# Kernel optimization log

Hardware: AMD Instinct MI355X
Metric: run time of the kernel (lower is better)

Reference implementation:

```python
import jax, jax.numpy as jnp
import numpy as np

B, O, T, C_IN, IMG, P, D = 16, 3, 8, 3, 224, 16, 768
HF = IMG // P  # 14x14 conv feature grid
S = 7          # ObjectsCrops output size (SxS per object per frame)


def setup_inputs() -> dict:
    key = jax.random.key(0)
    ks = jax.random.split(key, 6)
    x = jax.random.normal(ks[0], (B, C_IN, T, IMG, IMG), dtype=jnp.float32)
    # metadata: [B, O, T, 4] boxes (x1,y1,x2,y2) in pixel coords within [0,224]
    u = jax.random.uniform(ks[1], (B, O, T, 4), dtype=jnp.float32)
    bx1 = u[..., 0] * 160.0
    by1 = u[..., 1] * 160.0
    bw = 16.0 + u[..., 2] * 48.0
    bh = 16.0 + u[..., 3] * 48.0
    metadata = jnp.stack([bx1, by1, jnp.minimum(bx1 + bw, 224.0), jnp.minimum(by1 + bh, 224.0)], axis=-1)
    proj_w = jax.random.normal(ks[2], (D, C_IN, P, P), dtype=jnp.float32) * 0.02  # Conv3d kernel, tubelet dim (=1) squeezed
    proj_b = jnp.zeros((D,), dtype=jnp.float32)
    box_categories = jax.random.normal(ks[3], (T, O, D), dtype=jnp.float32) * 0.02
    w1 = jax.random.normal(ks[4], (4, D // 2), dtype=jnp.float32) * 0.1   # Linear(4, 384, bias=False)
    w2 = jax.random.normal(ks[5], (D // 2, D), dtype=jnp.float32) * 0.05  # Linear(384, 768, bias=False)
    return dict(x=x, metadata=metadata, proj_w=proj_w, proj_b=proj_b, box_categories=box_categories, w1=w1, w2=w2)


def _roi_crop(feat, boxes):
    # feat: [BT, C, Hf, Wf]; boxes: [BT, O, 4] (x1,y1,x2,y2) in feature-map coords
    BT, C, Hf, Wf = feat.shape
    x1, y1, x2, y2 = (boxes[..., i] for i in range(4))
    cell = (jnp.arange(S, dtype=feat.dtype) + 0.5) / S               # sample cell centers
    ys = y1[..., None] + cell * (y2 - y1)[..., None]                 # [BT,O,S]
    xs = x1[..., None] + cell * (x2 - x1)[..., None]
    yg = jnp.broadcast_to(ys[:, :, :, None], (BT, O, S, S)) - 0.5    # pixel centers at idx+0.5
    xg = jnp.broadcast_to(xs[:, :, None, :], (BT, O, S, S)) - 0.5
    y0f = jnp.floor(yg); x0f = jnp.floor(xg)
    wy = yg - y0f; wx = xg - x0f
    y0 = jnp.clip(y0f.astype(jnp.int32), 0, Hf - 1); y1i = jnp.clip(y0 + 1, 0, Hf - 1)
    x0 = jnp.clip(x0f.astype(jnp.int32), 0, Wf - 1); x1i = jnp.clip(x0 + 1, 0, Wf - 1)
    gather = jax.vmap(lambda fm, yy, xx: fm[:, yy, xx])              # [C,Hf,Wf],[O,S,S] -> [C,O,S,S]
    v00 = gather(feat, y0, x0); v01 = gather(feat, y0, x1i)
    v10 = gather(feat, y1i, x0); v11 = gather(feat, y1i, x1i)
    wy = wy[:, None]; wx = wx[:, None]                               # [BT,1,O,S,S]
    return (v00 * (1 - wy) * (1 - wx) + v01 * (1 - wy) * wx
            + v10 * wy * (1 - wx) + v11 * wy * wx)                   # [BT,C,O,S,S]


def reference(x, metadata, proj_w, proj_b, box_categories, w1, w2):
    Bs = x.shape[0]
    boxes = jnp.transpose(metadata, (0, 2, 1, 3))                    # [B,T,O,4] pixel coords
    # coordinate MLP on normalized boxes + per-(frame,object) category embedding
    box_emb = jax.nn.relu(jax.nn.relu((boxes / 224.0) @ w1) @ w2)    # [B,T,O,D]
    box_emb = box_categories[None] + box_emb
    # Conv3d patch embed: tubelet=1, stride==kernel -> non-overlapping patchify + GEMM
    xp = x.reshape(Bs, C_IN, T, HF, P, HF, P)
    feat = jnp.einsum('bcthpwq,dcpq->btdhw', xp, proj_w) + proj_b[None, None, :, None, None]
    feat = feat.reshape(Bs * T, D, HF, HF)
    fboxes = boxes.reshape(Bs * T, O, 4) * (HF / 224.0)              # boxes in feature coords
    crops = _roi_crop(feat, fboxes).reshape(Bs, T, D, O, S, S)
    xo = jnp.transpose(crops, (0, 3, 2, 1, 4, 5))                    # [B,O,C,T,S,S]
    emb = jnp.transpose(box_emb, (0, 2, 3, 1))                       # [B,O,D,T]
    xo = xo + emb[..., None, None]
    xo = xo.reshape(Bs * O, D, T, S * S)                             # flatten(3) on [N*O,C,T,H,W]
    return jnp.transpose(xo, (0, 2, 3, 1))                           # [B*O, T, S*S, D]
```

## Files before the change

kernel.cpp:

```cpp
#include <hip/hip_runtime.h>
#include <hip/hip_bf16.h>

typedef unsigned int u32;
typedef unsigned short ushort_t;
typedef __bf16 bf16x8 __attribute__((ext_vector_type(8)));
typedef float f32x4 __attribute__((ext_vector_type(4)));
typedef unsigned short ushort8 __attribute__((ext_vector_type(8)));

#define GM 25088
#define GK 768
#define GN 768

__device__ __forceinline__ ushort_t f2bf(float f) {
    u32 u = __float_as_uint(f);
    u32 r = (u + 0x7FFFu + ((u >> 16) & 1u)) >> 16;
    return (ushort_t)r;
}

__device__ __forceinline__ void load_lds16(const void* g, void* l) {
    __builtin_amdgcn_global_load_lds(
        (const __attribute__((address_space(1))) u32*)g,
        (__attribute__((address_space(3))) u32*)l, 16, 0, 0);
}

__global__ __launch_bounds__(256) void pack_a(const float* __restrict__ x,
                                              ushort_t* __restrict__ Ap) {
    int g = blockIdx.x * 256 + threadIdx.x;
    int w = g % 14;
    int rowg = g / 14;
    int row = rowg % 224;
    int bct = rowg / 224;
    int t = bct % 8;
    int bc = bct / 8;
    int c = bc % 3;
    int b = bc / 3;
    int p = row & 15;
    int h = row >> 4;
    const float* src = x + (size_t)g * 16;
    f32x4 f0 = *(const f32x4*)src;
    f32x4 f1 = *(const f32x4*)(src + 4);
    f32x4 f2 = *(const f32x4*)(src + 8);
    f32x4 f3 = *(const f32x4*)(src + 12);
    ushort8 r0, r1;
    r0[0] = f2bf(f0[0]); r0[1] = f2bf(f0[1]); r0[2] = f2bf(f0[2]); r0[3] = f2bf(f0[3]);
    r0[4] = f2bf(f1[0]); r0[5] = f2bf(f1[1]); r0[6] = f2bf(f1[2]); r0[7] = f2bf(f1[3]);
    r1[0] = f2bf(f2[0]); r1[1] = f2bf(f2[1]); r1[2] = f2bf(f2[2]); r1[3] = f2bf(f2[3]);
    r1[4] = f2bf(f3[0]); r1[5] = f2bf(f3[1]); r1[6] = f2bf(f3[2]); r1[7] = f2bf(f3[3]);
    int m = ((b * 8 + t) * 14 + h) * 14 + w;
    int k = c * 256 + p * 16;
    *(ushort8*)(Ap + (size_t)m * 768 + k) = r0;
    *(ushort8*)(Ap + (size_t)m * 768 + k + 8) = r1;
}

__global__ __launch_bounds__(256) void pack_w(const float* __restrict__ w,
                                              ushort_t* __restrict__ Wp) {
    size_t g = ((size_t)blockIdx.x * 256 + threadIdx.x) * 8;
    f32x4 f0 = *(const f32x4*)(w + g);
    f32x4 f1 = *(const f32x4*)(w + g + 4);
    ushort8 r;
    r[0] = f2bf(f0[0]); r[1] = f2bf(f0[1]); r[2] = f2bf(f0[2]); r[3] = f2bf(f0[3]);
    r[4] = f2bf(f1[0]); r[5] = f2bf(f1[1]); r[6] = f2bf(f1[2]); r[7] = f2bf(f1[3]);
    *(ushort8*)(Wp + g) = r;
}

__global__ __launch_bounds__(256) void box_mlp(const float* __restrict__ meta,
                                               const float* __restrict__ w1,
                                               const float* __restrict__ w2,
                                               const float* __restrict__ cats,
                                               float* __restrict__ emb) {
    int bt = blockIdx.x / 3;
    int dc = blockIdx.x % 3;
    int b = bt / 8, t = bt % 8;
    __shared__ float H[3][384];
    int tid = threadIdx.x;
    for (int idx = tid; idx < 3 * 384; idx += 256) {
        int o = idx / 384, j = idx % 384;
        const float* mp = meta + ((b * 3 + o) * 8 + t) * 4;
        float s = 0.f;
        #pragma unroll
        for (int i = 0; i < 4; ++i) s += (mp[i] * (1.0f / 224.0f)) * w1[i * 384 + j];
        H[o][j] = fmaxf(s, 0.f);
    }
    __syncthreads();
    int d = dc * 256 + tid;
    float acc[3] = {0.f, 0.f, 0.f};
    #pragma unroll 4
    for (int j = 0; j < 384; ++j) {
        float wv = w2[j * 768 + d];
        acc[0] += H[0][j] * wv;
        acc[1] += H[1][j] * wv;
        acc[2] += H[2][j] * wv;
    }
    #pragma unroll
    for (int o = 0; o < 3; ++o) {
        emb[((size_t)bt * 3 + o) * 768 + d] =
            fmaxf(acc[o], 0.f) + cats[(t * 3 + o) * 768 + d];
    }
}

__global__ __launch_bounds__(256) void gemm_bt(const ushort_t* __restrict__ A,
                                               const ushort_t* __restrict__ Bt,
                                               const float* __restrict__ pb,
                                               float* __restrict__ C) {
    __shared__ ushort_t lA[128 * 64];
    __shared__ ushort_t lB[128 * 64];
    int tid = threadIdx.x;
    int bid = blockIdx.x;
    int wid = (bid & 7) * 147 + (bid >> 3);
    int bm = wid / 6;
    int bn = wid % 6;
    size_t m0 = (size_t)bm * 128, n0 = (size_t)bn * 128;
    int w = tid >> 6, lane = tid & 63;
    int wr = w >> 1, wc = w & 1;

    f32x4 acc[4][4] = {};

    for (int kt = 0; kt < 12; ++kt) {
        int k0 = kt * 64;
        __syncthreads();
        #pragma unroll
        for (int r = 0; r < 4; ++r) {
            int cidx = r * 256 + tid;
            int row = cidx >> 3;
            int col = (cidx & 7) * 8;
            load_lds16(A + ((m0 + row) * 768 + k0 + col), &lA[(size_t)cidx * 8]);
        }
        #pragma unroll
        for (int r = 0; r < 4; ++r) {
            int cidx = r * 256 + tid;
            int row = cidx >> 3;
            int col = (cidx & 7) * 8;
            load_lds16(Bt + ((n0 + row) * 768 + k0 + col), &lB[(size_t)cidx * 8]);
        }
        __syncthreads();
        #pragma unroll
        for (int kk = 0; kk < 2; ++kk) {
            bf16x8 af[4], bfr[4];
            #pragma unroll
            for (int mi = 0; mi < 4; ++mi)
                af[mi] = *(const bf16x8*)&lA[(wr * 64 + mi * 16 + (lane & 15)) * 64
                                             + kk * 32 + (lane >> 4) * 8];
            #pragma unroll
            for (int ni = 0; ni < 4; ++ni)
                bfr[ni] = *(const bf16x8*)&lB[(wc * 64 + ni * 16 + (lane & 15)) * 64
                                              + kk * 32 + (lane >> 4) * 8];
            #pragma unroll
            for (int mi = 0; mi < 4; ++mi)
                #pragma unroll
                for (int ni = 0; ni < 4; ++ni)
                    acc[mi][ni] = __builtin_amdgcn_mfma_f32_16x16x32_bf16(
                        af[mi], bfr[ni], acc[mi][ni], 0, 0, 0);
        }
    }

    int rbase = (lane >> 4) * 4;
    int cl = lane & 15;
    #pragma unroll
    for (int ni = 0; ni < 4; ++ni) {
        size_t col = n0 + wc * 64 + ni * 16 + cl;
        float pbv = pb[col];
        #pragma unroll
        for (int mi = 0; mi < 4; ++mi) {
            size_t row = m0 + wr * 64 + mi * 16 + rbase;
            #pragma unroll
            for (int j = 0; j < 4; ++j) {
                C[(row + j) * 768 + col] = acc[mi][ni][j] + pbv;
            }
        }
    }
}

__global__ __launch_bounds__(192) void roi_kernel(const float* __restrict__ meta,
                                                  const float* __restrict__ feat,
                                                  const float* __restrict__ emb,
                                                  float* __restrict__ out) {
    int bid = blockIdx.x;
    int wid = (bid & 7) * 336 + (bid >> 3);
    int i = wid % 7; wid /= 7;
    int o = wid % 3; wid /= 3;
    int t = wid % 8;
    int b = wid / 8;

    const float* mp = meta + ((b * 3 + o) * 8 + t) * 4;
    float x1 = mp[0] * (1.f / 16.f);
    float y1 = mp[1] * (1.f / 16.f);
    float x2 = mp[2] * (1.f / 16.f);
    float y2 = mp[3] * (1.f / 16.f);

    float ci = (i + 0.5f) * (1.f / 7.f);
    float yg = y1 + ci * (y2 - y1) - 0.5f;
    float y0f = floorf(yg);
    float wy = yg - y0f;
    int y0 = min(max((int)y0f, 0), 13);
    int y1c = min(y0 + 1, 13);

    int bt = b * 8 + t;
    const float* fbase = feat + (size_t)bt * 196 * 768;
    const float* ep = emb + ((size_t)bt * 3 + o) * 768;

    int d = threadIdx.x * 4;
    f32x4 ev = *(const f32x4*)(ep + d);

    for (int j = 0; j < 7; ++j) {
        float cj = (j + 0.5f) * (1.f / 7.f);
        float xgv = x1 + cj * (x2 - x1) - 0.5f;
        float x0f = floorf(xgv);
        float wx = xgv - x0f;
        int x0 = min(max((int)x0f, 0), 13);
        int x1i = min(x0 + 1, 13);

        f32x4 v00 = *(const f32x4*)(fbase + ((size_t)y0 * 14 + x0) * 768 + d);
        f32x4 v01 = *(const f32x4*)(fbase + ((size_t)y0 * 14 + x1i) * 768 + d);
        f32x4 v10 = *(const f32x4*)(fbase + ((size_t)y1c * 14 + x0) * 768 + d);
        f32x4 v11 = *(const f32x4*)(fbase + ((size_t)y1c * 14 + x1i) * 768 + d);

        float w00 = (1.f - wy) * (1.f - wx);
        float w01 = (1.f - wy) * wx;
        float w10 = wy * (1.f - wx);
        float w11 = wy * wx;

        f32x4 r;
        #pragma unroll
        for (int e = 0; e < 4; ++e)
            r[e] = v00[e] * w00 + v01[e] * w01 + v10[e] * w10 + v11[e] * w11 + ev[e];

        int pp = i * 7 + j;
        *(f32x4*)(out + ((((size_t)(b * 3 + o) * 8 + t) * 49 + pp) * 768 + d)) = r;
    }
}

extern "C" void kernel_launch(void* const* d_in, const int* in_sizes, int n_in,
                              void* d_out, int out_size, void* d_ws, size_t ws_size,
                              hipStream_t stream) {
    const float* x     = (const float*)d_in[0];
    const float* meta  = (const float*)d_in[1];
    const float* projw = (const float*)d_in[2];
    const float* projb = (const float*)d_in[3];
    const float* cats  = (const float*)d_in[4];
    const float* w1    = (const float*)d_in[5];
    const float* w2    = (const float*)d_in[6];
    float* out = (float*)d_out;

    char* ws = (char*)d_ws;
    const size_t szA = (size_t)GM * GK * 2;
    const size_t szW = (size_t)GN * GK * 2;
    const size_t szF = (size_t)GM * GN * 4;
    ushort_t* Ap   = (ushort_t*)(ws);
    ushort_t* Wp   = (ushort_t*)(ws + szA);
    float*    feat = (float*)(ws + szA + szW);
    float*    emb  = (float*)(ws + szA + szW + szF);

    pack_a<<<4704, 256, 0, stream>>>(x, Ap);
    pack_w<<<288, 256, 0, stream>>>(projw, Wp);
    box_mlp<<<128 * 3, 256, 0, stream>>>(meta, w1, w2, cats, emb);
    gemm_bt<<<1176, 256, 0, stream>>>(Ap, Wp, projb, feat);
    roi_kernel<<<2688, 192, 0, stream>>>(meta, feat, emb, out);
}
```

Measured before the change: 270.5 us.

## Fuse prep kernels, double-buffer swizzled GEMM, store bf16 features, persistent ROI

```diff
diff --git a/kernel.cpp b/kernel.cpp
--- a/kernel.cpp
+++ b/kernel.cpp
@@ -6,6 +6,7 @@
 typedef __bf16 bf16x8 __attribute__((ext_vector_type(8)));
 typedef float f32x4 __attribute__((ext_vector_type(4)));
 typedef unsigned short ushort8 __attribute__((ext_vector_type(8)));
+typedef unsigned short ushort4v __attribute__((ext_vector_type(4)));
 
 #define GM 25088
 #define GK 768
@@ -17,93 +18,118 @@
     return (ushort_t)r;
 }
 
+__device__ __forceinline__ f32x4 bf2f4(ushort4v u) {
+    f32x4 f;
+    #pragma unroll
+    for (int e = 0; e < 4; ++e) f[e] = __uint_as_float(((u32)u[e]) << 16);
+    return f;
+}
+
 __device__ __forceinline__ void load_lds16(const void* g, void* l) {
     __builtin_amdgcn_global_load_lds(
         (const __attribute__((address_space(1))) u32*)g,
         (__attribute__((address_space(3))) u32*)l, 16, 0, 0);
 }
 
-__global__ __launch_bounds__(256) void pack_a(const float* __restrict__ x,
-                                              ushort_t* __restrict__ Ap) {
-    int g = blockIdx.x * 256 + threadIdx.x;
-    int w = g % 14;
-    int rowg = g / 14;
-    int row = rowg % 224;
-    int bct = rowg / 224;
-    int t = bct % 8;
-    int bc = bct / 8;
-    int c = bc % 3;
-    int b = bc / 3;
-    int p = row & 15;
-    int h = row >> 4;
-    const float* src = x + (size_t)g * 16;
-    f32x4 f0 = *(const f32x4*)src;
-    f32x4 f1 = *(const f32x4*)(src + 4);
-    f32x4 f2 = *(const f32x4*)(src + 8);
-    f32x4 f3 = *(const f32x4*)(src + 12);
-    ushort8 r0, r1;
-    r0[0] = f2bf(f0[0]); r0[1] = f2bf(f0[1]); r0[2] = f2bf(f0[2]); r0[3] = f2bf(f0[3]);
-    r0[4] = f2bf(f1[0]); r0[5] = f2bf(f1[1]); r0[6] = f2bf(f1[2]); r0[7] = f2bf(f1[3]);
-    r1[0] = f2bf(f2[0]); r1[1] = f2bf(f2[1]); r1[2] = f2bf(f2[2]); r1[3] = f2bf(f2[3]);
-    r1[4] = f2bf(f3[0]); r1[5] = f2bf(f3[1]); r1[6] = f2bf(f3[2]); r1[7] = f2bf(f3[3]);
-    int m = ((b * 8 + t) * 14 + h) * 14 + w;
-    int k = c * 256 + p * 16;
-    *(ushort8*)(Ap + (size_t)m * 768 + k) = r0;
-    *(ushort8*)(Ap + (size_t)m * 768 + k + 8) = r1;
-}
-
-__global__ __launch_bounds__(256) void pack_w(const float* __restrict__ w,
-                                              ushort_t* __restrict__ Wp) {
-    size_t g = ((size_t)blockIdx.x * 256 + threadIdx.x) * 8;
-    f32x4 f0 = *(const f32x4*)(w + g);
-    f32x4 f1 = *(const f32x4*)(w + g + 4);
-    ushort8 r;
-    r[0] = f2bf(f0[0]); r[1] = f2bf(f0[1]); r[2] = f2bf(f0[2]); r[3] = f2bf(f0[3]);
-    r[4] = f2bf(f1[0]); r[5] = f2bf(f1[1]); r[6] = f2bf(f1[2]); r[7] = f2bf(f1[3]);
-    *(ushort8*)(Wp + g) = r;
-}
-
-__global__ __launch_bounds__(256) void box_mlp(const float* __restrict__ meta,
-                                               const float* __restrict__ w1,
-                                               const float* __restrict__ w2,
-                                               const float* __restrict__ cats,
-                                               float* __restrict__ emb) {
-    int bt = blockIdx.x / 3;
-    int dc = blockIdx.x % 3;
-    int b = bt / 8, t = bt % 8;
+__global__ __launch_bounds__(256) void prep(const float* __restrict__ x,
+                                            const float* __restrict__ projw,
+                                            const float* __restrict__ meta,
+                                            const float* __restrict__ w1,
+                                            const float* __restrict__ w2,
+                                            const float* __restrict__ cats,
+                                            ushort_t* __restrict__ Ap,
+                                            ushort_t* __restrict__ Wp,
+                                            float* __restrict__ emb) {
     __shared__ float H[3][384];
+    int bid = blockIdx.x;
     int tid = threadIdx.x;
-    for (int idx = tid; idx < 3 * 384; idx += 256) {
-        int o = idx / 384, j = idx % 384;
-        const float* mp = meta + ((b * 3 + o) * 8 + t) * 4;
-        float s = 0.f;
-        #pragma unroll
-        for (int i = 0; i < 4; ++i) s += (mp[i] * (1.0f / 224.0f)) * w1[i * 384 + j];
-        H[o][j] = fmaxf(s, 0.f);
-    }
-    __syncthreads();
-    int d = dc * 256 + tid;
-    float acc[3] = {0.f, 0.f, 0.f};
-    #pragma unroll 4
-    for (int j = 0; j < 384; ++j) {
-        float wv = w2[j * 768 + d];
-        acc[0] += H[0][j] * wv;
-        acc[1] += H[1][j] * wv;
-        acc[2] += H[2][j] * wv;
-    }
-    #pragma unroll
-    for (int o = 0; o < 3; ++o) {
-        emb[((size_t)bt * 3 + o) * 768 + d] =
-            fmaxf(acc[o], 0.f) + cats[(t * 3 + o) * 768 + d];
+    if (bid < 1176) {
+        int g = bid * 256 + tid;
+        int m = g / 12;
+        int piece = g % 12;
+        int w = m % 14, h = (m / 14) % 14, t = (m / 196) % 8, b = m / 1568;
+        int c = piece >> 2, p0 = (piece & 3) * 4;
+        const float* src = x + ((size_t)((b * 3 + c) * 8 + t) * 224 + h * 16 + p0) * 224 + w * 16;
+        int xo = (m & 7) << 4;
+        ushort_t* dst = Ap + (size_t)m * 768 + piece * 64;
+        #pragma unroll
+        for (int i = 0; i < 4; ++i) {
+            const float* s = src + i * 224;
+            f32x4 f0 = *(const f32x4*)(s);
+            f32x4 f1 = *(const f32x4*)(s + 4);
+            f32x4 f2 = *(const f32x4*)(s + 8);
+            f32x4 f3 = *(const f32x4*)(s + 12);
+            ushort8 r0, r1;
+            r0[0] = f2bf(f0[0]); r0[1] = f2bf(f0[1]); r0[2] = f2bf(f0[2]); r0[3] = f2bf(f0[3]);
+            r0[4] = f2bf(f1[0]); r0[5] = f2bf(f1[1]); r0[6] = f2bf(f1[2]); r0[7] = f2bf(f1[3]);
+            r1[0] = f2bf(f2[0]); r1[1] = f2bf(f2[1]); r1[2] = f2bf(f2[2]); r1[3] = f2bf(f2[3]);
+            r1[4] = f2bf(f3[0]); r1[5] = f2bf(f3[1]); r1[6] = f2bf(f3[2]); r1[7] = f2bf(f3[3]);
+            int b0 = (i * 32) ^ xo;
+            int b1 = (i * 32 + 16) ^ xo;
+            *(ushort8*)(dst + (b0 >> 1)) = r0;
+            *(ushort8*)(dst + (b1 >> 1)) = r1;
+        }
+    } else if (bid < 1212) {
+        int g = (bid - 1176) * 256 + tid;
+        int n = g / 12;
+        int piece = g % 12;
+        const float* src = projw + (size_t)n * 768 + piece * 64;
+        int xo = (n & 7) << 4;
+        ushort_t* dst = Wp + (size_t)n * 768 + piece * 64;
+        #pragma unroll
+        for (int i = 0; i < 4; ++i) {
+            const float* s = src + i * 16;
+            f32x4 f0 = *(const f32x4*)(s);
+            f32x4 f1 = *(const f32x4*)(s + 4);
+            f32x4 f2 = *(const f32x4*)(s + 8);
+            f32x4 f3 = *(const f32x4*)(s + 12);
+            ushort8 r0, r1;
+            r0[0] = f2bf(f0[0]); r0[1] = f2bf(f0[1]); r0[2] = f2bf(f0[2]); r0[3] = f2bf(f0[3]);
+            r0[4] = f2bf(f1[0]); r0[5] = f2bf(f1[1]); r0[6] = f2bf(f1[2]); r0[7] = f2bf(f1[3]);
+            r1[0] = f2bf(f2[0]); r1[1] = f2bf(f2[1]); r1[2] = f2bf(f2[2]); r1[3] = f2bf(f2[3]);
+            r1[4] = f2bf(f3[0]); r1[5] = f2bf(f3[1]); r1[6] = f2bf(f3[2]); r1[7] = f2bf(f3[3]);
+            int b0 = (i * 32) ^ xo;
+            int b1 = (i * 32 + 16) ^ xo;
+            *(ushort8*)(dst + (b0 >> 1)) = r0;
+            *(ushort8*)(dst + (b1 >> 1)) = r1;
+        }
+    } else {
+        int bb = bid - 1212;
+        int bt = bb / 3;
+        int dc = bb % 3;
+        int b = bt / 8, t = bt % 8;
+        for (int idx = tid; idx < 3 * 384; idx += 256) {
+            int o = idx / 384, j = idx % 384;
+            const float* mp = meta + ((b * 3 + o) * 8 + t) * 4;
+            float s = 0.f;
+            #pragma unroll
+            for (int i = 0; i < 4; ++i) s += (mp[i] * (1.0f / 224.0f)) * w1[i * 384 + j];
+            H[o][j] = fmaxf(s, 0.f);
+        }
+        __syncthreads();
+        int d = dc * 256 + tid;
+        float acc[3] = {0.f, 0.f, 0.f};
+        #pragma unroll 4
+        for (int j = 0; j < 384; ++j) {
+            float wv = w2[j * 768 + d];
+            acc[0] += H[0][j] * wv;
+            acc[1] += H[1][j] * wv;
+            acc[2] += H[2][j] * wv;
+        }
+        #pragma unroll
+        for (int o = 0; o < 3; ++o) {
+            emb[((size_t)bt * 3 + o) * 768 + d] =
+                fmaxf(acc[o], 0.f) + cats[(t * 3 + o) * 768 + d];
+        }
     }
 }
 
 __global__ __launch_bounds__(256) void gemm_bt(const ushort_t* __restrict__ A,
                                                const ushort_t* __restrict__ Bt,
                                                const float* __restrict__ pb,
-                                               float* __restrict__ C) {
-    __shared__ ushort_t lA[128 * 64];
-    __shared__ ushort_t lB[128 * 64];
+                                               ushort_t* __restrict__ Cb) {
+    __shared__ ushort_t lA[2][128 * 64];
+    __shared__ ushort_t lB[2][128 * 64];
     int tid = threadIdx.x;
     int bid = blockIdx.x;
     int wid = (bid & 7) * 147 + (bid >> 3);
@@ -112,38 +138,46 @@
     size_t m0 = (size_t)bm * 128, n0 = (size_t)bn * 128;
     int w = tid >> 6, lane = tid & 63;
     int wr = w >> 1, wc = w & 1;
+    int r15 = lane & 15;
+    int xoU = (lane & 7) << 3;
 
     f32x4 acc[4][4] = {};
 
+    #define STAGE(buf, kt_)                                                        \
+        {                                                                          \
+            int k0_ = (kt_) * 64;                                                  \
+            _Pragma("unroll")                                                      \
+            for (int r = 0; r < 4; ++r) {                                          \
+                int cidx = r * 256 + tid;                                          \
+                int row = cidx >> 3;                                               \
+                int col = (cidx & 7) * 8;                                          \
+                load_lds16(A + ((m0 + row) * 768 + k0_ + col), &lA[buf][cidx * 8]);\
+            }                                                                      \
+            _Pragma("unroll")                                                      \
+            for (int r = 0; r < 4; ++r) {                                          \
+                int cidx = r * 256 + tid;                                          \
+                int row = cidx >> 3;                                               \
+                int col = (cidx & 7) * 8;                                          \
+                load_lds16(Bt + ((n0 + row) * 768 + k0_ + col), &lB[buf][cidx * 8]);\
+            }                                                                      \
+        }
+
+    STAGE(0, 0);
+    __syncthreads();
+
     for (int kt = 0; kt < 12; ++kt) {
-        int k0 = kt * 64;
-        __syncthreads();
-        #pragma unroll
-        for (int r = 0; r < 4; ++r) {
-            int cidx = r * 256 + tid;
-            int row = cidx >> 3;
-            int col = (cidx & 7) * 8;
-            load_lds16(A + ((m0 + row) * 768 + k0 + col), &lA[(size_t)cidx * 8]);
-        }
-        #pragma unroll
-        for (int r = 0; r < 4; ++r) {
-            int cidx = r * 256 + tid;
-            int row = cidx >> 3;
-            int col = (cidx & 7) * 8;
-            load_lds16(Bt + ((n0 + row) * 768 + k0 + col), &lB[(size_t)cidx * 8]);
-        }
-        __syncthreads();
+        int cur = kt & 1;
+        if (kt < 11) STAGE(cur ^ 1, kt + 1);
         #pragma unroll
         for (int kk = 0; kk < 2; ++kk) {
+            int cs = (kk * 32 + (lane >> 4) * 8) ^ xoU;
             bf16x8 af[4], bfr[4];
             #pragma unroll
             for (int mi = 0; mi < 4; ++mi)
-                af[mi] = *(const bf16x8*)&lA[(wr * 64 + mi * 16 + (lane & 15)) * 64
-                                             + kk * 32 + (lane >> 4) * 8];
+                af[mi] = *(const bf16x8*)&lA[cur][(wr * 64 + mi * 16 + r15) * 64 + cs];
             #pragma unroll
             for (int ni = 0; ni < 4; ++ni)
-                bfr[ni] = *(const bf16x8*)&lB[(wc * 64 + ni * 16 + (lane & 15)) * 64
-                                              + kk * 32 + (lane >> 4) * 8];
+                bfr[ni] = *(const bf16x8*)&lB[cur][(wc * 64 + ni * 16 + r15) * 64 + cs];
             #pragma unroll
             for (int mi = 0; mi < 4; ++mi)
                 #pragma unroll
@@ -151,81 +185,86 @@
                     acc[mi][ni] = __builtin_amdgcn_mfma_f32_16x16x32_bf16(
                         af[mi], bfr[ni], acc[mi][ni], 0, 0, 0);
         }
-    }
+        __syncthreads();
+    }
+    #undef STAGE
 
     int rbase = (lane >> 4) * 4;
-    int cl = lane & 15;
     #pragma unroll
     for (int ni = 0; ni < 4; ++ni) {
-        size_t col = n0 + wc * 64 + ni * 16 + cl;
+        size_t col = n0 + wc * 64 + ni * 16 + r15;
         float pbv = pb[col];
         #pragma unroll
         for (int mi = 0; mi < 4; ++mi) {
             size_t row = m0 + wr * 64 + mi * 16 + rbase;
             #pragma unroll
             for (int j = 0; j < 4; ++j) {
-                C[(row + j) * 768 + col] = acc[mi][ni][j] + pbv;
+                Cb[(row + j) * 768 + col] = f2bf(acc[mi][ni][j] + pbv);
             }
         }
     }
 }
 
 __global__ __launch_bounds__(192) void roi_kernel(const float* __restrict__ meta,
-                                                  const float* __restrict__ feat,
+                                                  const ushort_t* __restrict__ featB,
                                                   const float* __restrict__ emb,
                                                   float* __restrict__ out) {
-    int bid = blockIdx.x;
-    int wid = (bid & 7) * 336 + (bid >> 3);
-    int i = wid % 7; wid /= 7;
-    int o = wid % 3; wid /= 3;
-    int t = wid % 8;
-    int b = wid / 8;
-
-    const float* mp = meta + ((b * 3 + o) * 8 + t) * 4;
-    float x1 = mp[0] * (1.f / 16.f);
-    float y1 = mp[1] * (1.f / 16.f);
-    float x2 = mp[2] * (1.f / 16.f);
-    float y2 = mp[3] * (1.f / 16.f);
-
-    float ci = (i + 0.5f) * (1.f / 7.f);
-    float yg = y1 + ci * (y2 - y1) - 0.5f;
-    float y0f = floorf(yg);
-    float wy = yg - y0f;
-    int y0 = min(max((int)y0f, 0), 13);
-    int y1c = min(y0 + 1, 13);
-
-    int bt = b * 8 + t;
-    const float* fbase = feat + (size_t)bt * 196 * 768;
-    const float* ep = emb + ((size_t)bt * 3 + o) * 768;
-
+    int xcd = blockIdx.x & 7;
+    int idx = blockIdx.x >> 3;
     int d = threadIdx.x * 4;
-    f32x4 ev = *(const f32x4*)(ep + d);
-
-    for (int j = 0; j < 7; ++j) {
-        float cj = (j + 0.5f) * (1.f / 7.f);
-        float xgv = x1 + cj * (x2 - x1) - 0.5f;
-        float x0f = floorf(xgv);
-        float wx = xgv - x0f;
-        int x0 = min(max((int)x0f, 0), 13);
-        int x1i = min(x0 + 1, 13);
-
-        f32x4 v00 = *(const f32x4*)(fbase + ((size_t)y0 * 14 + x0) * 768 + d);
-        f32x4 v01 = *(const f32x4*)(fbase + ((size_t)y0 * 14 + x1i) * 768 + d);
-        f32x4 v10 = *(const f32x4*)(fbase + ((size_t)y1c * 14 + x0) * 768 + d);
-        f32x4 v11 = *(const f32x4*)(fbase + ((size_t)y1c * 14 + x1i) * 768 + d);
-
-        float w00 = (1.f - wy) * (1.f - wx);
-        float w01 = (1.f - wy) * wx;
-        float w10 = wy * (1.f - wx);
-        float w11 = wy * wx;
-
-        f32x4 r;
-        #pragma unroll
-        for (int e = 0; e < 4; ++e)
-            r[e] = v00[e] * w00 + v01[e] * w01 + v10[e] * w10 + v11[e] * w11 + ev[e];
-
-        int pp = i * 7 + j;
-        *(f32x4*)(out + ((((size_t)(b * 3 + o) * 8 + t) * 49 + pp) * 768 + d)) = r;
+
+    for (int wi = idx; wi < 336; wi += 96) {
+        int wid = xcd * 336 + wi;
+        int i = wid % 7; int r = wid / 7;
+        int o = r % 3; r /= 3;
+        int t = r % 8;
+        int b = r / 8;
+
+        const float* mp = meta + ((b * 3 + o) * 8 + t) * 4;
+        float x1 = mp[0] * (1.f / 16.f);
+        float y1 = mp[1] * (1.f / 16.f);
+        float x2 = mp[2] * (1.f / 16.f);
+        float y2 = mp[3] * (1.f / 16.f);
+
+        float ci = (i + 0.5f) * (1.f / 7.f);
+        float yg = y1 + ci * (y2 - y1) - 0.5f;
+        float y0f = floorf(yg);
+        float wy = yg - y0f;
+        int y0 = min(max((int)y0f, 0), 13);
+        int y1c = min(y0 + 1, 13);
+
+        int bt = b * 8 + t;
+        const ushort_t* fbase = featB + (size_t)bt * 196 * 768;
+        const float* ep = emb + ((size_t)bt * 3 + o) * 768;
+        f32x4 ev = *(const f32x4*)(ep + d);
+
+        #pragma unroll
+        for (int j = 0; j < 7; ++j) {
+            float cj = (j + 0.5f) * (1.f / 7.f);
+            float xgv = x1 + cj * (x2 - x1) - 0.5f;
+            float x0f = floorf(xgv);
+            float wx = xgv - x0f;
+            int x0 = min(max((int)x0f, 0), 13);
+            int x1i = min(x0 + 1, 13);
+
+            f32x4 v00 = bf2f4(*(const ushort4v*)(fbase + ((size_t)y0 * 14 + x0) * 768 + d));
+            f32x4 v01 = bf2f4(*(const ushort4v*)(fbase + ((size_t)y0 * 14 + x1i) * 768 + d));
+            f32x4 v10 = bf2f4(*(const ushort4v*)(fbase + ((size_t)y1c * 14 + x0) * 768 + d));
+            f32x4 v11 = bf2f4(*(const ushort4v*)(fbase + ((size_t)y1c * 14 + x1i) * 768 + d));
+
+            float w00 = (1.f - wy) * (1.f - wx);
+            float w01 = (1.f - wy) * wx;
+            float w10 = wy * (1.f - wx);
+            float w11 = wy * wx;
+
+            f32x4 rr;
+            #pragma unroll
+            for (int e = 0; e < 4; ++e)
+                rr[e] = v00[e] * w00 + v01[e] * w01 + v10[e] * w10 + v11[e] * w11 + ev[e];
+
+            int pp = i * 7 + j;
+            *(f32x4*)(out + ((((size_t)(b * 3 + o) * 8 + t) * 49 + pp) * 768 + d)) = rr;
+        }
     }
 }
 
@@ -242,17 +281,15 @@
     float* out = (float*)d_out;
 
     char* ws = (char*)d_ws;
-    const size_t szA = (size_t)GM * GK * 2;
-    const size_t szW = (size_t)GN * GK * 2;
-    const size_t szF = (size_t)GM * GN * 4;
-    ushort_t* Ap   = (ushort_t*)(ws);
-    ushort_t* Wp   = (ushort_t*)(ws + szA);
-    float*    feat = (float*)(ws + szA + szW);
-    float*    emb  = (float*)(ws + szA + szW + szF);
-
-    pack_a<<<4704, 256, 0, stream>>>(x, Ap);
-    pack_w<<<288, 256, 0, stream>>>(projw, Wp);
-    box_mlp<<<128 * 3, 256, 0, stream>>>(meta, w1, w2, cats, emb);
-    gemm_bt<<<1176, 256, 0, stream>>>(Ap, Wp, projb, feat);
-    roi_kernel<<<2688, 192, 0, stream>>>(meta, feat, emb, out);
-}
+    const size_t szA  = (size_t)GM * GK * 2;
+    const size_t szW  = (size_t)GN * GK * 2;
+    const size_t szFB = (size_t)GM * GN * 2;
+    ushort_t* Ap    = (ushort_t*)(ws);
+    ushort_t* Wp    = (ushort_t*)(ws + szA);
+    ushort_t* featB = (ushort_t*)(ws + szA + szW);
+    float*    emb   = (float*)(ws + szA + szW + szFB);
+
+    prep<<<1596, 256, 0, stream>>>(x, projw, meta, w1, w2, cats, Ap, Wp, emb);
+    gemm_bt<<<1176, 256, 0, stream>>>(Ap, Wp, projb, featB);
+    roi_kernel<<<768, 192, 0, stream>>>(meta, featB, emb, out);
+}
```

Result: faster. 245.5 us (-9.3%).
